# Performance work log

Measured on AMD Instinct MI355X. Metric: run time of the kernel, lower is better.

The kernel has to match this reference:

```python
import jax, jax.numpy as jnp
import numpy as np

N, D, HID, IN_DIM, ED = 8192, 16, 128, 128, 8


def _lin(k, fi, fo):
    return jax.random.normal(k, (fi, fo), jnp.float32) / np.sqrt(fi).astype(np.float32)


def setup_inputs() -> dict:
    key = jax.random.key(0)
    ks = jax.random.split(key, 8)
    rng = np.random.default_rng(0)
    # DAG with topological order 0..N-1: node v in [1,N) gets D predecessors in [0, v)
    v_arr = np.arange(1, N)
    src = np.floor(rng.random((N - 1, D)) * v_arr[:, None]).astype(np.int64)  # [N-1, D]
    dst = np.repeat(v_arr, D)
    edge_index = jnp.asarray(np.stack([src.reshape(-1), dst]))  # [2, E]
    E = (N - 1) * D
    return {
        "x": jax.random.normal(ks[0], (N, IN_DIM), jnp.float32),
        "edge_index": edge_index,
        "edge_attr": jax.random.normal(ks[1], (E, ED), jnp.float32),
        "Wp": _lin(ks[2], IN_DIM, HID), "bp": jnp.zeros(HID, jnp.float32),
        "Wm1": _lin(ks[3], HID + ED, HID), "bm1": jnp.zeros(HID, jnp.float32),
        "Wm2": _lin(ks[4], HID, HID), "bm2": jnp.zeros(HID, jnp.float32),
        "Wu1": _lin(ks[5], 2 * HID, HID), "bu1": jnp.zeros(HID, jnp.float32),
        "Wu2": _lin(ks[6], HID, HID), "bu2": jnp.zeros(HID, jnp.float32),
    }


def _build_struct(edge_index, num_nodes):
    # Group edges by destination, padded to max in-degree (host-side, int constants)
    si, di = np.asarray(edge_index)
    order = np.argsort(di, kind="stable")
    si_s, di_s = si[order], di[order]
    deg = np.bincount(di_s, minlength=num_nodes)
    Dm = max(int(deg.max()), 1)
    offs = np.concatenate([[0], np.cumsum(deg)])
    pos = np.arange(di_s.shape[0]) - offs[di_s]  # slot of each edge within its dst group
    src_pad = np.zeros((num_nodes, Dm), np.int64)
    mask = np.zeros((num_nodes, Dm), np.float32)
    src_pad[di_s, pos] = si_s
    mask[di_s, pos] = 1.0
    return (jnp.asarray(src_pad), jnp.asarray(mask),
            jnp.asarray(order), jnp.asarray(di_s), jnp.asarray(pos), Dm)


def _forward(x, edge_attr, params, struct):
    Wp, bp, Wm1, bm1, Wm2, bm2, Wu1, bu1, Wu2, bu2 = params
    src_pad, mask, order, di_s, pos, Dm = struct
    num_nodes = x.shape[0]
    relu = jax.nn.relu
    # Scatter edge attrs into padded [N, Dm, ED] slots (differentiable w.r.t. edge_attr)
    attr_pad = jnp.zeros((num_nodes, Dm, edge_attr.shape[-1]), edge_attr.dtype)
    attr_pad = attr_pad.at[di_s, pos].set(edge_attr[order])
    h0 = x @ Wp + bp  # node_proj

    def step(h, inp):
        srcs, attr, m, v = inp
        hs = h[srcs]                                    # [Dm, HID] current (possibly updated) states
        z = jnp.concatenate([hs, attr], axis=-1)        # [Dm, HID+ED]
        msgs = relu(relu(z @ Wm1 + bm1) @ Wm2 + bm2)    # msg_mlp
        cnt = m.sum()
        agg = (msgs * m[:, None]).sum(0) / jnp.maximum(cnt, 1.0)  # masked mean
        cat = jnp.concatenate([h[v], agg])              # [2*HID]
        new = relu(relu(cat @ Wu1 + bu1) @ Wu2 + bu2)   # update_mlp
        h = h.at[v].set(jnp.where(cnt > 0, new, h[v]))  # skip nodes with no in-edges
        return h, None

    h, _ = jax.lax.scan(step, h0, (src_pad, attr_pad, mask, jnp.arange(num_nodes)))
    return h


def reference(x, edge_index, edge_attr, Wp, bp, Wm1, bm1, Wm2, bm2, Wu1, bu1, Wu2, bu2):
    struct = _build_struct(edge_index, x.shape[0])
    params = (Wp, bp, Wm1, bm1, Wm2, bm2, Wu1, bu1, Wu2, bu2)
    return _forward(x, edge_attr, params, struct)
```

## Files before the change

### kernel.cpp

```cpp
#include <hip/hip_runtime.h>

#define NN   8192
#define DEG  16
#define HID  128
#define IND  128
#define ED   8
#define NBLK 256

typedef __bf16 bf16_t;
typedef __bf16 bf16x8 __attribute__((ext_vector_type(8)));
typedef float  f32x4  __attribute__((ext_vector_type(4)));
typedef unsigned long long u64;
typedef u64 u64x2 __attribute__((ext_vector_type(2)));

static __device__ __forceinline__ f32x4 mfma16(bf16x8 a, bf16x8 b, f32x4 c) {
  return __builtin_amdgcn_mfma_f32_16x16x32_bf16(a, b, c, 0, 0, 0);
}
static __device__ __forceinline__ unsigned short bfbits(bf16_t x) {
  return __builtin_bit_cast(unsigned short, x);
}
static __device__ __forceinline__ bf16_t bits2bf(unsigned short x) {
  return __builtin_bit_cast(bf16_t, x);
}
static __device__ __forceinline__ void bar_lds() {
  __builtin_amdgcn_sched_barrier(0);
  asm volatile("s_waitcnt lgkmcnt(0)" ::: "memory");
  __builtin_amdgcn_s_barrier();
  __builtin_amdgcn_sched_barrier(0);
}
static __device__ __forceinline__ void bar_full() {
  __builtin_amdgcn_sched_barrier(0);
  asm volatile("s_waitcnt vmcnt(0) lgkmcnt(0)" ::: "memory");
  __builtin_amdgcn_s_barrier();
  __builtin_amdgcn_sched_barrier(0);
}

__global__ __launch_bounds__(128) void k_h0(const float* __restrict__ x,
                                            const float* __restrict__ Wp,
                                            const float* __restrict__ bp,
                                            float* __restrict__ h,
                                            bf16_t* __restrict__ h2hi,
                                            bf16_t* __restrict__ h2lo,
                                            int* __restrict__ flags, int fs,
                                            int sent) {
  __shared__ float sx[8][IND];
  const int t  = threadIdx.x;
  const int vb = blockIdx.x * 8;
  #pragma unroll
  for (int rr = 0; rr < 8; ++rr) sx[rr][t] = x[(size_t)(vb + rr) * IND + t];
  __syncthreads();
  float acc[8];
  const float bias = bp[t];
  #pragma unroll
  for (int rr = 0; rr < 8; ++rr) acc[rr] = bias;
  for (int k = 0; k < IND; ++k) {
    const float w = Wp[k * HID + t];
    #pragma unroll
    for (int rr = 0; rr < 8; ++rr) acc[rr] += sx[rr][k] * w;
  }
  #pragma unroll
  for (int rr = 0; rr < 8; ++rr) h[(size_t)(vb + rr) * HID + t] = acc[rr];
  if (sent) {
    #pragma unroll
    for (int rr = 0; rr < 8; ++rr) {
      unsigned short hw = 0xFFFFu, lw = 0xFFFFu;
      if (vb + rr == 0) {
        const float f = acc[rr];
        const bf16_t fh = (bf16_t)f;
        hw = bfbits(fh);
        lw = bfbits((bf16_t)(f - (float)fh));
      }
      h2hi[(size_t)(vb + rr) * HID + t] = bits2bf(hw);
      h2lo[(size_t)(vb + rr) * HID + t] = bits2bf(lw);
    }
  } else if (t < 8) {
    flags[(vb + t) * fs] = (vb + t == 0) ? 0xF : 0;
  }
}

#define LOAD_WFRAGS(W, KROWS, NKK, ARRH, ARRL)                                \
  _Pragma("unroll")                                                           \
  for (int n = 0; n < 2; ++n) {                                               \
    _Pragma("unroll")                                                         \
    for (int kk = 0; kk < NKK; ++kk) {                                        \
      _Pragma("unroll")                                                       \
      for (int i = 0; i < 8; ++i) {                                           \
        const int k = kk * 32 + g * 8 + i;                                    \
        const float w = (k < KROWS) ? W[k * HID + cc[n]] : 0.f;               \
        const bf16_t wh = (bf16_t)w;                                          \
        ARRH[n][kk][i] = wh;                                                  \
        ARRL[n][kk][i] = (bf16_t)(w - (float)wh);                             \
      }                                                                       \
    }                                                                         \
  }
#define LOAD_WFRAGS_H(W, KROWS, NKK, ARRH)                                    \
  _Pragma("unroll")                                                           \
  for (int n = 0; n < 2; ++n) {                                               \
    _Pragma("unroll")                                                         \
    for (int kk = 0; kk < NKK; ++kk) {                                        \
      _Pragma("unroll")                                                       \
      for (int i = 0; i < 8; ++i) {                                           \
        const int k = kk * 32 + g * 8 + i;                                    \
        const float w = (k < KROWS) ? W[k * HID + cc[n]] : 0.f;               \
        ARRH[n][kk][i] = (bf16_t)w;                                           \
      }                                                                       \
    }                                                                         \
  }
#define LOAD_WFRAGS_L(W, KROWS, NKK, ARRL)                                    \
  _Pragma("unroll")                                                           \
  for (int n = 0; n < 2; ++n) {                                               \
    _Pragma("unroll")                                                         \
    for (int kk = 0; kk < NKK; ++kk) {                                        \
      _Pragma("unroll")                                                       \
      for (int i = 0; i < 8; ++i) {                                           \
        const int k = kk * 32 + g * 8 + i;                                    \
        const float w = (k < KROWS) ? W[k * HID + cc[n]] : 0.f;               \
        ARRL[n][kk][i] = (bf16_t)(w - (float)(bf16_t)w);                      \
      }                                                                       \
    }                                                                         \
  }

#define LOADQH()                                                              \
  _Pragma("unroll")                                                           \
  for (int kk = 0; kk < 4; ++kk) {                                            \
    _Pragma("unroll")                                                         \
    for (int u = 0; u < 2; ++u)                                               \
      q[kk * 2 + u] = __hip_atomic_load(hp + kk * 8 + u, __ATOMIC_RELAXED,    \
                                        __HIP_MEMORY_SCOPE_AGENT);            \
  }

#define ZERO4(a) { a[0][0]=0.f;a[0][1]=0.f;a[0][2]=0.f;a[0][3]=0.f; a[1]=a[0]; }
#define BIAS4(a, b) { a[0][0]=b[0];a[0][1]=b[0];a[0][2]=b[0];a[0][3]=b[0];    \
                      a[1][0]=b[1];a[1][1]=b[1];a[1][2]=b[1];a[1][3]=b[1]; }

template <bool SENT>
__global__ __launch_bounds__(256, 1) void k_dag(
    const int* __restrict__ ei, const float* __restrict__ attr,
    const float* __restrict__ Wm1, const float* __restrict__ bm1,
    const float* __restrict__ Wm2, const float* __restrict__ bm2,
    const float* __restrict__ Wu1, const float* __restrict__ bu1,
    const float* __restrict__ Wu2, const float* __restrict__ bu2,
    float* __restrict__ h, bf16_t* __restrict__ h2hi,
    bf16_t* __restrict__ h2lo, int* __restrict__ flags, int fs) {
  const int tid  = threadIdx.x;
  const int lane = tid & 63;
  const int g    = lane >> 4;
  const int r    = lane & 15;
  const int wid  = tid >> 6;

  __shared__ bf16_t s_m1[16 * HID];
  __shared__ alignas(16) bf16_t s_agg[HID];
  __shared__ alignas(16) bf16_t s_u1[HID];

  int cc[2];
  cc[0] = wid * 32 + 2 * r;
  cc[1] = cc[0] + 1;

  bf16x8 wm1h[2][5], wm1l[2][5];
  bf16x8 wm2h[2][4];
  bf16x8 wu1h[2][8], wu1l[2][4];
  bf16x8 wu2h[2][4], wu2l[2][4];
  LOAD_WFRAGS(Wm1, 136, 5, wm1h, wm1l)
  LOAD_WFRAGS_H(Wm2, 128, 4, wm2h)
  LOAD_WFRAGS_H(Wu1, 256, 8, wu1h)
  LOAD_WFRAGS_L(Wu1, 128, 4, wu1l)
  LOAD_WFRAGS(Wu2, 128, 4, wu2h, wu2l)
  float bs_m1[2], bs_m2[2], bs_u1[2], bs_u2[2];
  #pragma unroll
  for (int n = 0; n < 2; ++n) {
    bs_m1[n] = bm1[cc[n]]; bs_m2[n] = bm2[cc[n]];
    bs_u1[n] = bu1[cc[n]]; bs_u2[n] = bu2[cc[n]];
  }

  const int v0 = 1 + (int)blockIdx.x;
  int s_cur = (v0 < NN) ? ei[(v0 - 1) * DEG + r] : 0;

  for (int v = v0; v < NN; v += NBLK) {
    u64 q[16];
    const u64* hp;
    if constexpr (SENT) {
      hp = (const u64*)(h2hi + (size_t)s_cur * HID) + g * 2;
      LOADQH();
    } else {
      hp = (const u64*)(h + (size_t)s_cur * HID) + g * 4;
      #pragma unroll
      for (int kk = 0; kk < 4; ++kk)
        #pragma unroll
        for (int u = 0; u < 4; ++u)
          q[kk * 4 + u] = __hip_atomic_load(hp + kk * 16 + u, __ATOMIC_RELAXED,
                                            __HIP_MEMORY_SCOPE_AGENT);
    }

    const int vn = (v + NBLK < NN) ? v + NBLK : v;
    const int s_nxt = ei[(vn - 1) * DEG + r];

    bf16x8 hvh[4], hvl[4];
    {
      const float* hvp = h + (size_t)v * HID + g * 8;
      #pragma unroll
      for (int kk = 0; kk < 4; ++kk) {
        const f32x4 p0 = *(const f32x4*)(hvp + kk * 32);
        const f32x4 p1 = *(const f32x4*)(hvp + kk * 32 + 4);
        #pragma unroll
        for (int i = 0; i < 4; ++i) {
          const float f0 = p0[i], f1 = p1[i];
          const bf16_t f0h = (bf16_t)f0, f1h = (bf16_t)f1;
          hvh[kk][i]     = f0h; hvl[kk][i]     = (bf16_t)(f0 - (float)f0h);
          hvh[kk][4 + i] = f1h; hvl[kk][4 + i] = (bf16_t)(f1 - (float)f1h);
        }
      }
    }
    bf16x8 a4h;
    #pragma unroll
    for (int i = 0; i < 8; ++i) a4h[i] = (bf16_t)0.f;
    if (g == 0) {
      const f32x4* ap = (const f32x4*)(attr + ((size_t)(v - 1) * DEG + r) * ED);
      const f32x4 a0 = ap[0], a1 = ap[1];
      #pragma unroll
      for (int i = 0; i < 4; ++i) {
        a4h[i] = (bf16_t)a0[i]; a4h[4 + i] = (bf16_t)a1[i];
      }
    }

    f32x4 uA[2], uB[2], uC[2], uD[2];
    BIAS4(uA, bs_u1) ZERO4(uB) ZERO4(uC) ZERO4(uD)
    #pragma unroll
    for (int kk = 0; kk < 4; ++kk) {
      #pragma unroll
      for (int n = 0; n < 2; ++n) {
        uA[n] = mfma16(hvh[kk], wu1h[n][kk], uA[n]);
        uB[n] = mfma16(hvh[kk], wu1l[n][kk], uB[n]);
        uC[n] = mfma16(hvl[kk], wu1h[n][kk], uC[n]);
      }
    }
    f32x4 mA[2], mB[2], mD[2], mE[2];
    BIAS4(mA, bs_m1) ZERO4(mB) ZERO4(mD) ZERO4(mE)
    #pragma unroll
    for (int n = 0; n < 2; ++n) {
      mA[n] = mfma16(a4h, wm1h[n][4], mA[n]);
      mB[n] = mfma16(a4h, wm1l[n][4], mB[n]);
    }

    if constexpr (SENT) {
      bool ok = false;
      int guard = 0;
      for (;;) {
        if (!ok) {
          u64 m = 0;
          #pragma unroll
          for (int i = 0; i < 8; ++i) m |= q[i];
          ok = (s_cur == 0) || ((m & 0x8000800080008000ull) == 0);
        }
        if (__all(ok)) break;
        if (++guard > (1 << 13)) break;
        if (!ok) LOADQH();
      }
    } else {
      const int* fp = flags + s_cur * fs;
      int fw = __hip_atomic_load(fp, __ATOMIC_RELAXED, __HIP_MEMORY_SCOPE_AGENT);
      int guard = 0;
      while (fw != 0xF && ++guard < (1 << 15)) {
        __builtin_amdgcn_s_sleep(1);
        fw = __hip_atomic_load(fp, __ATOMIC_RELAXED, __HIP_MEMORY_SCOPE_AGENT);
      }
      asm volatile("" ::: "memory");
      #pragma unroll
      for (int kk = 0; kk < 4; ++kk)
        #pragma unroll
        for (int u = 0; u < 4; ++u)
          q[kk * 4 + u] = __hip_atomic_load(hp + kk * 16 + u, __ATOMIC_RELAXED,
                                            __HIP_MEMORY_SCOPE_AGENT);
    }

    bf16x8 ah[4];
    #pragma unroll
    for (int kk = 0; kk < 4; ++kk) {
      if constexpr (SENT) {
        u64x2 t2; t2[0] = q[kk * 2]; t2[1] = q[kk * 2 + 1];
        ah[kk] = __builtin_bit_cast(bf16x8, t2);
      } else {
        #pragma unroll
        for (int u = 0; u < 4; ++u)
          #pragma unroll
          for (int b = 0; b < 2; ++b)
            ah[kk][u * 2 + b] =
                (bf16_t)__uint_as_float((unsigned)(q[kk * 4 + u] >> (32 * b)));
      }
    }

    f32x4 m1[2];
    #pragma unroll
    for (int kk = 0; kk < 2; ++kk) {
      #pragma unroll
      for (int n = 0; n < 2; ++n) {
        mA[n] = mfma16(ah[kk], wm1h[n][kk], mA[n]);
        mB[n] = mfma16(ah[kk], wm1l[n][kk], mB[n]);
        mD[n] = mfma16(ah[kk + 2], wm1h[n][kk + 2], mD[n]);
        mE[n] = mfma16(ah[kk + 2], wm1l[n][kk + 2], mE[n]);
      }
    }
    #pragma unroll
    for (int n = 0; n < 2; ++n) m1[n] = (mA[n] + mB[n]) + (mD[n] + mE[n]);
    #pragma unroll
    for (int n = 0; n < 2; ++n) {
      const int c = cc[n], ch16 = c >> 3;
      #pragma unroll
      for (int reg = 0; reg < 4; ++reg) {
        const int j = g * 4 + reg;
        s_m1[j * HID + ((ch16 ^ j) * 8) + (c & 7)] = (bf16_t)fmaxf(m1[n][reg], 0.f);
      }
    }
    if constexpr (SENT) bar_lds(); else __syncthreads();

    f32x4 m2[2];
    {
      f32x4 aA[2], aC[2];
      BIAS4(aA, bs_m2) ZERO4(aC)
      #pragma unroll
      for (int kk = 0; kk < 2; ++kk) {
        const int ph0 = (kk * 4 + g) ^ r;
        const int ph1 = ((kk + 2) * 4 + g) ^ r;
        const bf16x8 a0 = *(const bf16x8*)(s_m1 + r * HID + ph0 * 8);
        const bf16x8 a1 = *(const bf16x8*)(s_m1 + r * HID + ph1 * 8);
        #pragma unroll
        for (int n = 0; n < 2; ++n) {
          aA[n] = mfma16(a0, wm2h[n][kk], aA[n]);
          aC[n] = mfma16(a1, wm2h[n][kk + 2], aC[n]);
        }
      }
      #pragma unroll
      for (int n = 0; n < 2; ++n) m2[n] = aA[n] + aC[n];
    }
    #pragma unroll
    for (int n = 0; n < 2; ++n) {
      float s = fmaxf(m2[n][0],0.f)+fmaxf(m2[n][1],0.f)+fmaxf(m2[n][2],0.f)+fmaxf(m2[n][3],0.f);
      s += __shfl_xor(s, 16, 64);
      s += __shfl_xor(s, 32, 64);
      if (lane < 16) s_agg[cc[n]] = (bf16_t)(s * 0.0625f);
    }
    if constexpr (SENT) bar_lds(); else __syncthreads();

    f32x4 u1v[2];
    #pragma unroll
    for (int kk = 4; kk < 6; ++kk) {
      const bf16x8 Ah0 = *(const bf16x8*)(s_agg + (kk - 4) * 32 + g * 8);
      const bf16x8 Ah1 = *(const bf16x8*)(s_agg + (kk - 2) * 32 + g * 8);
      #pragma unroll
      for (int n = 0; n < 2; ++n) {
        uA[n] = mfma16(Ah0, wu1h[n][kk], uA[n]);
        uD[n] = mfma16(Ah1, wu1h[n][kk + 2], uD[n]);
      }
    }
    #pragma unroll
    for (int n = 0; n < 2; ++n)
      u1v[n] = (uA[n] + uB[n]) + (uC[n] + uD[n]);
    if (lane < 16) {
      s_u1[cc[0]] = (bf16_t)fmaxf(u1v[0][0], 0.f);
      s_u1[cc[1]] = (bf16_t)fmaxf(u1v[1][0], 0.f);
    }
    if constexpr (SENT) bar_lds(); else __syncthreads();

    f32x4 u2v[2];
    {
      f32x4 aA[2], aB[2], aC[2], aD[2];
      BIAS4(aA, bs_u2) ZERO4(aB) ZERO4(aC) ZERO4(aD)
      #pragma unroll
      for (int kk = 0; kk < 2; ++kk) {
        const bf16x8 Ah0 = *(const bf16x8*)(s_u1 + kk * 32 + g * 8);
        const bf16x8 Ah1 = *(const bf16x8*)(s_u1 + (kk + 2) * 32 + g * 8);
        #pragma unroll
        for (int n = 0; n < 2; ++n) {
          aA[n] = mfma16(Ah0, wu2h[n][kk], aA[n]);
          aB[n] = mfma16(Ah0, wu2l[n][kk], aB[n]);
          aC[n] = mfma16(Ah1, wu2h[n][kk + 2], aC[n]);
          aD[n] = mfma16(Ah1, wu2l[n][kk + 2], aD[n]);
        }
      }
      #pragma unroll
      for (int n = 0; n < 2; ++n) u2v[n] = (aA[n] + aB[n]) + (aC[n] + aD[n]);
    }
    if (lane < 16) {
      if constexpr (SENT) {
        const float r0 = fabsf(fmaxf(u2v[0][0], 0.f));
        const float r1 = fabsf(fmaxf(u2v[1][0], 0.f));
        const bf16_t h0b = (bf16_t)r0, h1b = (bf16_t)r1;
        const unsigned hiw = (unsigned)bfbits(h0b) | ((unsigned)bfbits(h1b) << 16);
        const unsigned low = (unsigned)bfbits((bf16_t)(r0 - (float)h0b)) |
                             ((unsigned)bfbits((bf16_t)(r1 - (float)h1b)) << 16);
        const size_t wi = (size_t)v * (HID / 2) + wid * 16 + r;
        __hip_atomic_store((unsigned*)h2lo + wi, low,
                           __ATOMIC_RELAXED, __HIP_MEMORY_SCOPE_AGENT);
        __hip_atomic_store((unsigned*)h2hi + wi, hiw,
                           __ATOMIC_RELAXED, __HIP_MEMORY_SCOPE_AGENT);
      } else {
        #pragma unroll
        for (int n = 0; n < 2; ++n) {
          const float rv = fabsf(fmaxf(u2v[n][0], 0.f));
          __hip_atomic_store(&h[(size_t)v * HID + cc[n]], rv,
                             __ATOMIC_RELAXED, __HIP_MEMORY_SCOPE_AGENT);
        }
      }
    }
    if constexpr (!SENT) {
      if (lane == 0)
        __hip_atomic_fetch_or(&flags[v * fs], 1 << wid, __ATOMIC_RELEASE,
                              __HIP_MEMORY_SCOPE_AGENT);
    }
    s_cur = s_nxt;
    if constexpr (!SENT) __syncthreads();
  }

  if constexpr (SENT) {
    bar_full();
    const unsigned* hi32 = (const unsigned*)h2hi;
    const unsigned* lo32 = (const unsigned*)h2lo;
    const int sub = tid >> 6;
    const int c2  = tid & 63;
    for (int v = v0 + sub * NBLK; v < NN; v += 4 * NBLK) {
      const unsigned hw = __hip_atomic_load(&hi32[(size_t)v * 64 + c2],
                                            __ATOMIC_RELAXED,
                                            __HIP_MEMORY_SCOPE_AGENT);
      const unsigned lw = __hip_atomic_load(&lo32[(size_t)v * 64 + c2],
                                            __ATOMIC_RELAXED,
                                            __HIP_MEMORY_SCOPE_AGENT);
      h[(size_t)v * HID + 2 * c2] =
          (float)bits2bf((unsigned short)(hw & 0xFFFF)) +
          (float)bits2bf((unsigned short)(lw & 0xFFFF));
      h[(size_t)v * HID + 2 * c2 + 1] =
          (float)bits2bf((unsigned short)(hw >> 16)) +
          (float)bits2bf((unsigned short)(lw >> 16));
    }
  }
}

extern "C" void kernel_launch(void* const* d_in, const int* in_sizes, int n_in,
                              void* d_out, int out_size, void* d_ws, size_t ws_size,
                              hipStream_t stream) {
  const float* x    = (const float*)d_in[0];
  const int*   ei   = (const int*)  d_in[1];
  const float* attr = (const float*)d_in[2];
  const float* Wp   = (const float*)d_in[3];
  const float* bp   = (const float*)d_in[4];
  const float* Wm1  = (const float*)d_in[5];
  const float* bm1  = (const float*)d_in[6];
  const float* Wm2  = (const float*)d_in[7];
  const float* bm2  = (const float*)d_in[8];
  const float* Wu1  = (const float*)d_in[9];
  const float* bu1  = (const float*)d_in[10];
  const float* Wu2  = (const float*)d_in[11];
  const float* bu2  = (const float*)d_in[12];
  float* h = (float*)d_out;

  const size_t plane = (size_t)NN * HID * sizeof(bf16_t);
  const bool sent = ws_size >= 2 * plane;
  bf16_t* h2hi = (bf16_t*)d_ws;
  bf16_t* h2lo = (bf16_t*)((char*)d_ws + plane);
  int* flags   = (int*)d_ws;
  const int fs = sent ? 0 : ((ws_size >= (size_t)NN * 64 + 64) ? 16 : 1);

  k_h0<<<NN / 8, 128, 0, stream>>>(x, Wp, bp, h, h2hi, h2lo, flags, fs,
                                   sent ? 1 : 0);
  if (sent)
    k_dag<true><<<NBLK, 256, 0, stream>>>(ei, attr, Wm1, bm1, Wm2, bm2,
                                          Wu1, bu1, Wu2, bu2, h, h2hi, h2lo,
                                          flags, fs);
  else
    k_dag<false><<<NBLK, 256, 0, stream>>>(ei, attr, Wm1, bm1, Wm2, bm2,
                                           Wu1, bu1, Wu2, bu2, h, h2hi, h2lo,
                                           flags, fs);
}
```

Before: 508.5 us.

## Drop bf16 low-plane state, write fp32 output directly, widen MFMA accumulator chains

The sentinel path no longer keeps a second bf16 'lo' plane of node states. Each node's fp32 result is written straight into the output, and only a bf16 'hi' copy is published for dependent nodes to poll. This removes the low-plane stores, the sentinel initialisation of that plane, and the final pass that rebuilt fp32 output from both planes. The MFMA reductions for the message and update MLPs are split into more independent accumulators to shorten dependency chains. The risks are lost precision in the neighbour states now gathered as bf16 only, and higher register pressure from the extra accumulators.

```diff
diff --git a/kernel.cpp b/kernel.cpp
--- a/kernel.cpp
+++ b/kernel.cpp
@@ -10,6 +10,7 @@
 typedef __bf16 bf16_t;
 typedef __bf16 bf16x8 __attribute__((ext_vector_type(8)));
 typedef float  f32x4  __attribute__((ext_vector_type(4)));
+typedef float  f32x2  __attribute__((ext_vector_type(2)));
 typedef unsigned long long u64;
 typedef u64 u64x2 __attribute__((ext_vector_type(2)));
 
@@ -28,19 +29,12 @@
   __builtin_amdgcn_s_barrier();
   __builtin_amdgcn_sched_barrier(0);
 }
-static __device__ __forceinline__ void bar_full() {
-  __builtin_amdgcn_sched_barrier(0);
-  asm volatile("s_waitcnt vmcnt(0) lgkmcnt(0)" ::: "memory");
-  __builtin_amdgcn_s_barrier();
-  __builtin_amdgcn_sched_barrier(0);
-}
 
 __global__ __launch_bounds__(128) void k_h0(const float* __restrict__ x,
                                             const float* __restrict__ Wp,
                                             const float* __restrict__ bp,
                                             float* __restrict__ h,
                                             bf16_t* __restrict__ h2hi,
-                                            bf16_t* __restrict__ h2lo,
                                             int* __restrict__ flags, int fs,
                                             int sent) {
   __shared__ float sx[8][IND];
@@ -63,15 +57,9 @@
   if (sent) {
     #pragma unroll
     for (int rr = 0; rr < 8; ++rr) {
-      unsigned short hw = 0xFFFFu, lw = 0xFFFFu;
-      if (vb + rr == 0) {
-        const float f = acc[rr];
-        const bf16_t fh = (bf16_t)f;
-        hw = bfbits(fh);
-        lw = bfbits((bf16_t)(f - (float)fh));
-      }
+      unsigned short hw = 0xFFFFu;
+      if (vb + rr == 0) hw = bfbits((bf16_t)acc[rr]);
       h2hi[(size_t)(vb + rr) * HID + t] = bits2bf(hw);
-      h2lo[(size_t)(vb + rr) * HID + t] = bits2bf(lw);
     }
   } else if (t < 8) {
     flags[(vb + t) * fs] = (vb + t == 0) ? 0xF : 0;
@@ -141,7 +129,7 @@
     const float* __restrict__ Wu1, const float* __restrict__ bu1,
     const float* __restrict__ Wu2, const float* __restrict__ bu2,
     float* __restrict__ h, bf16_t* __restrict__ h2hi,
-    bf16_t* __restrict__ h2lo, int* __restrict__ flags, int fs) {
+    int* __restrict__ flags, int fs) {
   const int tid  = threadIdx.x;
   const int lane = tid & 63;
   const int g    = lane >> 4;
@@ -233,8 +221,9 @@
         uC[n] = mfma16(hvl[kk], wu1h[n][kk], uC[n]);
       }
     }
-    f32x4 mA[2], mB[2], mD[2], mE[2];
-    BIAS4(mA, bs_m1) ZERO4(mB) ZERO4(mD) ZERO4(mE)
+    f32x4 mA[2], mB[2], mC[2], mD[2], mE[2], mF[2], mG[2], mH[2];
+    BIAS4(mA, bs_m1) ZERO4(mB) ZERO4(mC) ZERO4(mD)
+    ZERO4(mE) ZERO4(mF) ZERO4(mG) ZERO4(mH)
     #pragma unroll
     for (int n = 0; n < 2; ++n) {
       mA[n] = mfma16(a4h, wm1h[n][4], mA[n]);
@@ -290,17 +279,20 @@
 
     f32x4 m1[2];
     #pragma unroll
-    for (int kk = 0; kk < 2; ++kk) {
-      #pragma unroll
-      for (int n = 0; n < 2; ++n) {
-        mA[n] = mfma16(ah[kk], wm1h[n][kk], mA[n]);
-        mB[n] = mfma16(ah[kk], wm1l[n][kk], mB[n]);
-        mD[n] = mfma16(ah[kk + 2], wm1h[n][kk + 2], mD[n]);
-        mE[n] = mfma16(ah[kk + 2], wm1l[n][kk + 2], mE[n]);
-      }
-    }
-    #pragma unroll
-    for (int n = 0; n < 2; ++n) m1[n] = (mA[n] + mB[n]) + (mD[n] + mE[n]);
+    for (int n = 0; n < 2; ++n) {
+      mA[n] = mfma16(ah[0], wm1h[n][0], mA[n]);
+      mB[n] = mfma16(ah[1], wm1h[n][1], mB[n]);
+      mC[n] = mfma16(ah[2], wm1h[n][2], mC[n]);
+      mD[n] = mfma16(ah[3], wm1h[n][3], mD[n]);
+      mE[n] = mfma16(ah[0], wm1l[n][0], mE[n]);
+      mF[n] = mfma16(ah[1], wm1l[n][1], mF[n]);
+      mG[n] = mfma16(ah[2], wm1l[n][2], mG[n]);
+      mH[n] = mfma16(ah[3], wm1l[n][3], mH[n]);
+    }
+    #pragma unroll
+    for (int n = 0; n < 2; ++n)
+      m1[n] = ((mA[n] + mB[n]) + (mC[n] + mD[n])) +
+              ((mE[n] + mF[n]) + (mG[n] + mH[n]));
     #pragma unroll
     for (int n = 0; n < 2; ++n) {
       const int c = cc[n], ch16 = c >> 3;
@@ -314,22 +306,21 @@
 
     f32x4 m2[2];
     {
-      f32x4 aA[2], aC[2];
-      BIAS4(aA, bs_m2) ZERO4(aC)
-      #pragma unroll
-      for (int kk = 0; kk < 2; ++kk) {
-        const int ph0 = (kk * 4 + g) ^ r;
-        const int ph1 = ((kk + 2) * 4 + g) ^ r;
-        const bf16x8 a0 = *(const bf16x8*)(s_m1 + r * HID + ph0 * 8);
-        const bf16x8 a1 = *(const bf16x8*)(s_m1 + r * HID + ph1 * 8);
-        #pragma unroll
-        for (int n = 0; n < 2; ++n) {
-          aA[n] = mfma16(a0, wm2h[n][kk], aA[n]);
-          aC[n] = mfma16(a1, wm2h[n][kk + 2], aC[n]);
-        }
-      }
-      #pragma unroll
-      for (int n = 0; n < 2; ++n) m2[n] = aA[n] + aC[n];
+      f32x4 aA[2], aB[2], aC[2], aD[2];
+      BIAS4(aA, bs_m2) ZERO4(aB) ZERO4(aC) ZERO4(aD)
+      const bf16x8 a0 = *(const bf16x8*)(s_m1 + r * HID + (((0 * 4 + g) ^ r) * 8));
+      const bf16x8 a1 = *(const bf16x8*)(s_m1 + r * HID + (((1 * 4 + g) ^ r) * 8));
+      const bf16x8 a2 = *(const bf16x8*)(s_m1 + r * HID + (((2 * 4 + g) ^ r) * 8));
+      const bf16x8 a3 = *(const bf16x8*)(s_m1 + r * HID + (((3 * 4 + g) ^ r) * 8));
+      #pragma unroll
+      for (int n = 0; n < 2; ++n) {
+        aA[n] = mfma16(a0, wm2h[n][0], aA[n]);
+        aB[n] = mfma16(a1, wm2h[n][1], aB[n]);
+        aC[n] = mfma16(a2, wm2h[n][2], aC[n]);
+        aD[n] = mfma16(a3, wm2h[n][3], aD[n]);
+      }
+      #pragma unroll
+      for (int n = 0; n < 2; ++n) m2[n] = (aA[n] + aB[n]) + (aC[n] + aD[n]);
     }
     #pragma unroll
     for (int n = 0; n < 2; ++n) {
@@ -341,14 +332,17 @@
     if constexpr (SENT) bar_lds(); else __syncthreads();
 
     f32x4 u1v[2];
-    #pragma unroll
-    for (int kk = 4; kk < 6; ++kk) {
-      const bf16x8 Ah0 = *(const bf16x8*)(s_agg + (kk - 4) * 32 + g * 8);
-      const bf16x8 Ah1 = *(const bf16x8*)(s_agg + (kk - 2) * 32 + g * 8);
+    {
+      const bf16x8 A0 = *(const bf16x8*)(s_agg + 0 * 32 + g * 8);
+      const bf16x8 A1 = *(const bf16x8*)(s_agg + 1 * 32 + g * 8);
+      const bf16x8 A2 = *(const bf16x8*)(s_agg + 2 * 32 + g * 8);
+      const bf16x8 A3 = *(const bf16x8*)(s_agg + 3 * 32 + g * 8);
       #pragma unroll
       for (int n = 0; n < 2; ++n) {
-        uA[n] = mfma16(Ah0, wu1h[n][kk], uA[n]);
-        uD[n] = mfma16(Ah1, wu1h[n][kk + 2], uD[n]);
+        uA[n] = mfma16(A0, wu1h[n][4], uA[n]);
+        uB[n] = mfma16(A1, wu1h[n][5], uB[n]);
+        uC[n] = mfma16(A2, wu1h[n][6], uC[n]);
+        uD[n] = mfma16(A3, wu1h[n][7], uD[n]);
       }
     }
     #pragma unroll
@@ -362,43 +356,44 @@
 
     f32x4 u2v[2];
     {
-      f32x4 aA[2], aB[2], aC[2], aD[2];
+      f32x4 aA[2], aB[2], aC[2], aD[2], aE[2], aF[2], aG[2], aH[2];
       BIAS4(aA, bs_u2) ZERO4(aB) ZERO4(aC) ZERO4(aD)
-      #pragma unroll
-      for (int kk = 0; kk < 2; ++kk) {
-        const bf16x8 Ah0 = *(const bf16x8*)(s_u1 + kk * 32 + g * 8);
-        const bf16x8 Ah1 = *(const bf16x8*)(s_u1 + (kk + 2) * 32 + g * 8);
-        #pragma unroll
-        for (int n = 0; n < 2; ++n) {
-          aA[n] = mfma16(Ah0, wu2h[n][kk], aA[n]);
-          aB[n] = mfma16(Ah0, wu2l[n][kk], aB[n]);
-          aC[n] = mfma16(Ah1, wu2h[n][kk + 2], aC[n]);
-          aD[n] = mfma16(Ah1, wu2l[n][kk + 2], aD[n]);
-        }
-      }
-      #pragma unroll
-      for (int n = 0; n < 2; ++n) u2v[n] = (aA[n] + aB[n]) + (aC[n] + aD[n]);
+      ZERO4(aE) ZERO4(aF) ZERO4(aG) ZERO4(aH)
+      const bf16x8 A0 = *(const bf16x8*)(s_u1 + 0 * 32 + g * 8);
+      const bf16x8 A1 = *(const bf16x8*)(s_u1 + 1 * 32 + g * 8);
+      const bf16x8 A2 = *(const bf16x8*)(s_u1 + 2 * 32 + g * 8);
+      const bf16x8 A3 = *(const bf16x8*)(s_u1 + 3 * 32 + g * 8);
+      #pragma unroll
+      for (int n = 0; n < 2; ++n) {
+        aA[n] = mfma16(A0, wu2h[n][0], aA[n]);
+        aB[n] = mfma16(A1, wu2h[n][1], aB[n]);
+        aC[n] = mfma16(A2, wu2h[n][2], aC[n]);
+        aD[n] = mfma16(A3, wu2h[n][3], aD[n]);
+        aE[n] = mfma16(A0, wu2l[n][0], aE[n]);
+        aF[n] = mfma16(A1, wu2l[n][1], aF[n]);
+        aG[n] = mfma16(A2, wu2l[n][2], aG[n]);
+        aH[n] = mfma16(A3, wu2l[n][3], aH[n]);
+      }
+      #pragma unroll
+      for (int n = 0; n < 2; ++n)
+        u2v[n] = ((aA[n] + aB[n]) + (aC[n] + aD[n])) +
+                 ((aE[n] + aF[n]) + (aG[n] + aH[n]));
     }
     if (lane < 16) {
+      const float r0 = fabsf(fmaxf(u2v[0][0], 0.f));
+      const float r1 = fabsf(fmaxf(u2v[1][0], 0.f));
       if constexpr (SENT) {
-        const float r0 = fabsf(fmaxf(u2v[0][0], 0.f));
-        const float r1 = fabsf(fmaxf(u2v[1][0], 0.f));
-        const bf16_t h0b = (bf16_t)r0, h1b = (bf16_t)r1;
-        const unsigned hiw = (unsigned)bfbits(h0b) | ((unsigned)bfbits(h1b) << 16);
-        const unsigned low = (unsigned)bfbits((bf16_t)(r0 - (float)h0b)) |
-                             ((unsigned)bfbits((bf16_t)(r1 - (float)h1b)) << 16);
-        const size_t wi = (size_t)v * (HID / 2) + wid * 16 + r;
-        __hip_atomic_store((unsigned*)h2lo + wi, low,
+        const unsigned hiw = (unsigned)bfbits((bf16_t)r0) |
+                             ((unsigned)bfbits((bf16_t)r1) << 16);
+        __hip_atomic_store((unsigned*)h2hi + (size_t)v * (HID / 2) + wid * 16 + r,
+                           hiw, __ATOMIC_RELAXED, __HIP_MEMORY_SCOPE_AGENT);
+        f32x2 out2; out2[0] = r0; out2[1] = r1;
+        *(f32x2*)&h[(size_t)v * HID + cc[0]] = out2;
+      } else {
+        __hip_atomic_store(&h[(size_t)v * HID + cc[0]], r0,
                            __ATOMIC_RELAXED, __HIP_MEMORY_SCOPE_AGENT);
-        __hip_atomic_store((unsigned*)h2hi + wi, hiw,
+        __hip_atomic_store(&h[(size_t)v * HID + cc[1]], r1,
                            __ATOMIC_RELAXED, __HIP_MEMORY_SCOPE_AGENT);
-      } else {
-        #pragma unroll
-        for (int n = 0; n < 2; ++n) {
-          const float rv = fabsf(fmaxf(u2v[n][0], 0.f));
-          __hip_atomic_store(&h[(size_t)v * HID + cc[n]], rv,
-                             __ATOMIC_RELAXED, __HIP_MEMORY_SCOPE_AGENT);
-        }
       }
     }
     if constexpr (!SENT) {
@@ -408,28 +403,6 @@
     }
     s_cur = s_nxt;
     if constexpr (!SENT) __syncthreads();
-  }
-
-  if constexpr (SENT) {
-    bar_full();
-    const unsigned* hi32 = (const unsigned*)h2hi;
-    const unsigned* lo32 = (const unsigned*)h2lo;
-    const int sub = tid >> 6;
-    const int c2  = tid & 63;
-    for (int v = v0 + sub * NBLK; v < NN; v += 4 * NBLK) {
-      const unsigned hw = __hip_atomic_load(&hi32[(size_t)v * 64 + c2],
-                                            __ATOMIC_RELAXED,
-                                            __HIP_MEMORY_SCOPE_AGENT);
-      const unsigned lw = __hip_atomic_load(&lo32[(size_t)v * 64 + c2],
-                                            __ATOMIC_RELAXED,
-                                            __HIP_MEMORY_SCOPE_AGENT);
-      h[(size_t)v * HID + 2 * c2] =
-          (float)bits2bf((unsigned short)(hw & 0xFFFF)) +
-          (float)bits2bf((unsigned short)(lw & 0xFFFF));
-      h[(size_t)v * HID + 2 * c2 + 1] =
-          (float)bits2bf((unsigned short)(hw >> 16)) +
-          (float)bits2bf((unsigned short)(lw >> 16));
-    }
   }
 }
 
@@ -452,20 +425,18 @@
   float* h = (float*)d_out;
 
   const size_t plane = (size_t)NN * HID * sizeof(bf16_t);
-  const bool sent = ws_size >= 2 * plane;
+  const bool sent = ws_size >= plane;
   bf16_t* h2hi = (bf16_t*)d_ws;
-  bf16_t* h2lo = (bf16_t*)((char*)d_ws + plane);
   int* flags   = (int*)d_ws;
   const int fs = sent ? 0 : ((ws_size >= (size_t)NN * 64 + 64) ? 16 : 1);
 
-  k_h0<<<NN / 8, 128, 0, stream>>>(x, Wp, bp, h, h2hi, h2lo, flags, fs,
-                                   sent ? 1 : 0);
+  k_h0<<<NN / 8, 128, 0, stream>>>(x, Wp, bp, h, h2hi, flags, fs, sent ? 1 : 0);
   if (sent)
     k_dag<true><<<NBLK, 256, 0, stream>>>(ei, attr, Wm1, bm1, Wm2, bm2,
-                                          Wu1, bu1, Wu2, bu2, h, h2hi, h2lo,
+                                          Wu1, bu1, Wu2, bu2, h, h2hi,
                                           flags, fs);
   else
     k_dag<false><<<NBLK, 256, 0, stream>>>(ei, attr, Wm1, bm1, Wm2, bm2,
-                                           Wu1, bu1, Wu2, bu2, h, h2hi, h2lo,
+                                           Wu1, bu1, Wu2, bu2, h, h2hi,
                                            flags, fs);
 }
```

After: 508.9 us. Within noise of the previous version (+0.1%).
